# Performance work log

Hardware: AMD Instinct MI355X
Metric: run time of the kernel (lower is better)

Reference implementation:

```python
import jax, jax.numpy as jnp
import numpy as np

N = 50000      # nodes
E = 800000     # edges
P = 200000     # link pairs
D_IN = 128     # input_dim
F_NUM = 128    # filter_num
OUT = 2        # out_dim
K = 10         # APPNP propagation steps
ALPHA = 0.1    # teleport prob


def setup_inputs() -> dict:
    key = jax.random.key(0)
    ks = jax.random.split(key, 9)
    x = jax.random.normal(ks[0], (N, D_IN), dtype=jnp.float32)
    edge_index = jax.random.randint(ks[1], (2, E), 0, N)
    index = jax.random.randint(ks[2], (P, 2), 0, N)
    s1 = 1.0 / np.sqrt(D_IN)
    s2 = 1.0 / np.sqrt(F_NUM)
    s3 = 1.0 / np.sqrt(2 * F_NUM)
    W1 = jax.random.uniform(ks[3], (F_NUM, D_IN), minval=-s1, maxval=s1)
    b1 = jax.random.uniform(ks[4], (F_NUM,), minval=-s1, maxval=s1)
    W2 = jax.random.uniform(ks[5], (F_NUM, F_NUM), minval=-s2, maxval=s2)
    b2 = jax.random.uniform(ks[6], (F_NUM,), minval=-s2, maxval=s2)
    W3 = jax.random.uniform(ks[7], (OUT, 2 * F_NUM), minval=-s3, maxval=s3)
    b3 = jax.random.uniform(ks[8], (OUT,), minval=-s3, maxval=s3)
    return {"x": x, "edge_index": edge_index, "index": index,
            "W1": W1, "b1": b1, "W2": W2, "b2": b2, "W3": W3, "b3": b3}


def _gcn_norm(edge_index, num_nodes):
    # PyG gcn_norm: add self-loops, sym norm D^{-1/2} (A+I) D^{-1/2}
    src, dst = edge_index[0], edge_index[1]
    loop = jnp.arange(num_nodes, dtype=src.dtype)
    src = jnp.concatenate([src, loop])
    dst = jnp.concatenate([dst, loop])
    deg = jax.ops.segment_sum(jnp.ones_like(src, dtype=jnp.float32), dst,
                              num_segments=num_nodes)
    dinv = jnp.where(deg > 0, jax.lax.rsqrt(deg), 0.0)
    norm = dinv[src] * dinv[dst]  # [E+N]
    return src, dst, norm


def _appnp(x, src, dst, norm, num_nodes):
    # h_{k+1} = (1-alpha) * A_hat h_k + alpha * x0
    def step(h, _):
        agg = jax.ops.segment_sum(norm[:, None] * h[src], dst,
                                  num_segments=num_nodes)
        return (1.0 - ALPHA) * agg + ALPHA * x, None
    h, _ = jax.lax.scan(step, x, None, length=K)
    return h


def reference(x, edge_index, index, W1, b1, W2, b2, W3, b3):
    num_nodes = x.shape[0]
    src, dst, norm = _gcn_norm(edge_index, num_nodes)
    h = x @ W1.T + b1                      # [N, F]
    h = jax.nn.relu(_appnp(h, src, dst, norm, num_nodes))
    h = h @ W2.T + b2                      # [N, F]
    h = jax.nn.relu(_appnp(h, src, dst, norm, num_nodes))
    feat = jnp.concatenate([h[index[:, 0]], h[index[:, 1]]], axis=-1)  # [P, 2F]
    out = feat @ W3.T + b3                 # [P, OUT]
    return jax.nn.log_softmax(out, axis=1)
```

## Files before the change

### kernel.cpp

```cpp
#include <hip/hip_runtime.h>
#include <math.h>

#define NN 50000
#define NE 800000
#define NP 200000
#define NF 128
#define NEDGE_TOT (NE + NN)
#define NBLK 196

typedef __attribute__((ext_vector_type(8))) short short8;
typedef __attribute__((ext_vector_type(4))) float float4v;

__device__ __forceinline__ float bf_lo(unsigned u) { return __uint_as_float(u << 16); }
__device__ __forceinline__ float bf_hi(unsigned u) { return __uint_as_float(u & 0xffff0000u); }
__device__ __forceinline__ unsigned short f2bf(float f) {
    unsigned u = __float_as_uint(f);
    return (unsigned short)((u + 0x7fffu + ((u >> 16) & 1u)) >> 16);
}
__device__ __forceinline__ unsigned pack2bf(float a, float b) {
    return (unsigned)f2bf(a) | ((unsigned)f2bf(b) << 16);
}

__global__ __launch_bounds__(256) void init_cnt_k(int* __restrict__ cnt) {
    int i = blockIdx.x * 256 + threadIdx.x;
    if (i < NN) cnt[i] = 1;
}

__global__ __launch_bounds__(256) void count_k(const int* __restrict__ ei,
                                               int* __restrict__ cnt) {
    int e = blockIdx.x * 256 + threadIdx.x;
    if (e < NE) atomicAdd(&cnt[ei[NE + e]], 1);
}

__global__ __launch_bounds__(256) void scan_reduce_k(const int* __restrict__ cnt,
                                                     int* __restrict__ bsum,
                                                     float* __restrict__ dinv) {
    __shared__ int s[256];
    int t = threadIdx.x;
    int idx = blockIdx.x * 256 + t;
    int v = (idx < NN) ? cnt[idx] : 0;
    if (idx < NN) dinv[idx] = rsqrtf((float)v);
    s[t] = v;
    __syncthreads();
    for (int off = 128; off > 0; off >>= 1) {
        if (t < off) s[t] += s[t + off];
        __syncthreads();
    }
    if (t == 0) bsum[blockIdx.x] = s[0];
}

__global__ __launch_bounds__(256) void scan_bsums_k(const int* __restrict__ bsum,
                                                    int* __restrict__ boff) {
    __shared__ int s[256];
    int t = threadIdx.x;
    int v = (t < NBLK) ? bsum[t] : 0;
    s[t] = v;
    __syncthreads();
    for (int off = 1; off < 256; off <<= 1) {
        int add = (t >= off) ? s[t - off] : 0;
        __syncthreads();
        s[t] += add;
        __syncthreads();
    }
    if (t < NBLK) boff[t] = s[t] - v;
}

__global__ __launch_bounds__(256) void scan_down_k(const int* __restrict__ cnt,
                                                   const int* __restrict__ boff,
                                                   int* __restrict__ row_ptr,
                                                   int* __restrict__ wptr) {
    __shared__ int s[256];
    int t = threadIdx.x;
    int idx = blockIdx.x * 256 + t;
    int v = (idx < NN) ? cnt[idx] : 0;
    s[t] = v;
    __syncthreads();
    for (int off = 1; off < 256; off <<= 1) {
        int add = (t >= off) ? s[t - off] : 0;
        __syncthreads();
        s[t] += add;
        __syncthreads();
    }
    int excl = s[t] - v + boff[blockIdx.x];
    if (idx < NN) {
        row_ptr[idx] = excl;
        wptr[idx] = excl;
        if (idx == NN - 1) row_ptr[NN] = excl + v;
    }
}

__global__ __launch_bounds__(256) void scatter_k(const int* __restrict__ ei,
                                                 const float* __restrict__ dinv,
                                                 int* __restrict__ wptr,
                                                 int2* __restrict__ rec) {
    int e = blockIdx.x * 256 + threadIdx.x;
    if (e >= NEDGE_TOT) return;
    int s, d;
    if (e < NE) { s = ei[e]; d = ei[NE + e]; }
    else        { s = d = e - NE; }
    int pos = atomicAdd(&wptr[d], 1);
    int2 r;
    r.x = s;
    r.y = __float_as_int(dinv[s] * dinv[d]);
    rec[pos] = r;
}

__global__ __launch_bounds__(256) void cast_x_k(const float* __restrict__ x,
                                                unsigned short* __restrict__ Xb) {
    int t = blockIdx.x * 256 + threadIdx.x;
    if (t >= NN * 16) return;
    int i = t * 8;
    float4 f0 = *(const float4*)(x + i);
    float4 f1 = *(const float4*)(x + i + 4);
    uint4 q;
    q.x = pack2bf(f0.x, f0.y);
    q.y = pack2bf(f0.z, f0.w);
    q.z = pack2bf(f1.x, f1.y);
    q.w = pack2bf(f1.z, f1.w);
    *(uint4*)(Xb + i) = q;
}

__global__ __launch_bounds__(256) void cast_w_k(const float* __restrict__ W,
                                                unsigned short* __restrict__ Wb) {
    int t = blockIdx.x * 256 + threadIdx.x;
    if (t >= 128 * 128 / 8) return;
    int i = t * 8;
    float4 f0 = *(const float4*)(W + i);
    float4 f1 = *(const float4*)(W + i + 4);
    uint4 q;
    q.x = pack2bf(f0.x, f0.y);
    q.y = pack2bf(f0.z, f0.w);
    q.z = pack2bf(f1.x, f1.y);
    q.w = pack2bf(f1.z, f1.w);
    *(uint4*)(Wb + i) = q;
}

#define GPAD 136
__global__ __launch_bounds__(256) void gemm_mfma_k(const unsigned short* __restrict__ Xb,
                                                   const unsigned short* __restrict__ Wb,
                                                   const float* __restrict__ bias,
                                                   unsigned short* __restrict__ Yb,
                                                   int nrows) {
    __shared__ unsigned short sm[4 * 16 * GPAD];
    int wave = threadIdx.x >> 6, lane = threadIdx.x & 63;
    int rbase = blockIdx.x * 64 + wave * 16;
    if (rbase >= nrows) return;
    int quad = lane >> 4, mn = lane & 15;
    float4v acc[8];
#pragma unroll
    for (int ft = 0; ft < 8; ++ft) acc[ft] = (float4v){0.f, 0.f, 0.f, 0.f};
#pragma unroll
    for (int kb = 0; kb < 128; kb += 32) {
        short8 a = *(const short8*)(Xb + (size_t)(rbase + mn) * NF + kb + quad * 8);
#pragma unroll
        for (int ft = 0; ft < 8; ++ft) {
            short8 b = *(const short8*)(Wb + (size_t)(ft * 16 + mn) * NF + kb + quad * 8);
            acc[ft] = __builtin_amdgcn_mfma_f32_16x16x32_bf16(a, b, acc[ft], 0, 0, 0);
        }
    }
    unsigned short* smw = sm + wave * 16 * GPAD;
#pragma unroll
    for (int ft = 0; ft < 8; ++ft) {
        float bv = bias[ft * 16 + mn];
#pragma unroll
        for (int r = 0; r < 4; ++r)
            smw[(quad * 4 + r) * GPAD + ft * 16 + mn] = f2bf(acc[ft][r] + bv);
    }
    __syncthreads();
#pragma unroll
    for (int t = 0; t < 4; ++t) {
        int rl = t * 4 + quad;
        uint4 q = *(const uint4*)(smw + rl * GPAD + mn * 8);
        *(uint4*)(Yb + (size_t)(rbase + rl) * NF + mn * 8) = q;
    }
}

__global__ __launch_bounds__(256) void appnp4_k(const unsigned short* __restrict__ h,
                                                const unsigned short* __restrict__ x0,
                                                unsigned short* __restrict__ out,
                                                const int* __restrict__ row_ptr,
                                                const int2* __restrict__ rec,
                                                int relu, int proj,
                                                const float* __restrict__ W3,
                                                float4* __restrict__ puv) {
    int wid = (blockIdx.x * 256 + threadIdx.x) >> 6;
    int lane = threadIdx.x & 63;
    if (wid >= NN) return;
    int g = lane >> 4, li = lane & 15;
    int beg = row_ptr[wid], end = row_ptr[wid + 1];
    float a0 = 0.f, a1 = 0.f, a2 = 0.f, a3 = 0.f;
    float a4 = 0.f, a5 = 0.f, a6 = 0.f, a7 = 0.f;
    for (int e = beg; e < end; e += 64) {
        int m = end - e;
        if (m > 64) m = 64;
        int c = 0;
        float w = 0.f;
        if (lane < m) { int2 q = rec[e + lane]; c = q.x; w = __int_as_float(q.y); }
        for (int j = 0; j < m; j += 4) {
            int src = j + g;
            int cj = __shfl(c, src, 64);
            float wj = __shfl(w, src, 64);
            if (src < m) {
                uint4 q = *((const uint4*)(h + (size_t)cj * NF) + li);
                a0 += wj * bf_lo(q.x);
                a1 += wj * bf_hi(q.x);
                a2 += wj * bf_lo(q.y);
                a3 += wj * bf_hi(q.y);
                a4 += wj * bf_lo(q.z);
                a5 += wj * bf_hi(q.z);
                a6 += wj * bf_lo(q.w);
                a7 += wj * bf_hi(q.w);
            }
        }
    }
#pragma unroll
    for (int off = 16; off < 64; off <<= 1) {
        a0 += __shfl_xor(a0, off, 64);
        a1 += __shfl_xor(a1, off, 64);
        a2 += __shfl_xor(a2, off, 64);
        a3 += __shfl_xor(a3, off, 64);
        a4 += __shfl_xor(a4, off, 64);
        a5 += __shfl_xor(a5, off, 64);
        a6 += __shfl_xor(a6, off, 64);
        a7 += __shfl_xor(a7, off, 64);
    }
    if (g == 0) {
        uint4 xq = *((const uint4*)(x0 + (size_t)wid * NF) + li);
        float r0 = 0.9f * a0 + 0.1f * bf_lo(xq.x);
        float r1 = 0.9f * a1 + 0.1f * bf_hi(xq.x);
        float r2 = 0.9f * a2 + 0.1f * bf_lo(xq.y);
        float r3 = 0.9f * a3 + 0.1f * bf_hi(xq.y);
        float r4 = 0.9f * a4 + 0.1f * bf_lo(xq.z);
        float r5 = 0.9f * a5 + 0.1f * bf_hi(xq.z);
        float r6 = 0.9f * a6 + 0.1f * bf_lo(xq.w);
        float r7 = 0.9f * a7 + 0.1f * bf_hi(xq.w);
        if (relu) {
            r0 = fmaxf(r0, 0.f); r1 = fmaxf(r1, 0.f);
            r2 = fmaxf(r2, 0.f); r3 = fmaxf(r3, 0.f);
            r4 = fmaxf(r4, 0.f); r5 = fmaxf(r5, 0.f);
            r6 = fmaxf(r6, 0.f); r7 = fmaxf(r7, 0.f);
        }
        if (!proj) {
            uint4 oq;
            oq.x = pack2bf(r0, r1);
            oq.y = pack2bf(r2, r3);
            oq.z = pack2bf(r4, r5);
            oq.w = pack2bf(r6, r7);
            *((uint4*)(out + (size_t)wid * NF) + li) = oq;
        } else {
            int fb = li * 8;
            float4 wu0a = *(const float4*)(W3 + fb);
            float4 wu0b = *(const float4*)(W3 + fb + 4);
            float4 wv0a = *(const float4*)(W3 + 128 + fb);
            float4 wv0b = *(const float4*)(W3 + 128 + fb + 4);
            float4 wu1a = *(const float4*)(W3 + 256 + fb);
            float4 wu1b = *(const float4*)(W3 + 256 + fb + 4);
            float4 wv1a = *(const float4*)(W3 + 384 + fb);
            float4 wv1b = *(const float4*)(W3 + 384 + fb + 4);
            float du0 = r0 * wu0a.x + r1 * wu0a.y + r2 * wu0a.z + r3 * wu0a.w
                      + r4 * wu0b.x + r5 * wu0b.y + r6 * wu0b.z + r7 * wu0b.w;
            float du1 = r0 * wu1a.x + r1 * wu1a.y + r2 * wu1a.z + r3 * wu1a.w
                      + r4 * wu1b.x + r5 * wu1b.y + r6 * wu1b.z + r7 * wu1b.w;
            float dv0 = r0 * wv0a.x + r1 * wv0a.y + r2 * wv0a.z + r3 * wv0a.w
                      + r4 * wv0b.x + r5 * wv0b.y + r6 * wv0b.z + r7 * wv0b.w;
            float dv1 = r0 * wv1a.x + r1 * wv1a.y + r2 * wv1a.z + r3 * wv1a.w
                      + r4 * wv1b.x + r5 * wv1b.y + r6 * wv1b.z + r7 * wv1b.w;
#pragma unroll
            for (int off = 1; off < 16; off <<= 1) {
                du0 += __shfl_xor(du0, off, 64);
                du1 += __shfl_xor(du1, off, 64);
                dv0 += __shfl_xor(dv0, off, 64);
                dv1 += __shfl_xor(dv1, off, 64);
            }
            if (li == 0) puv[wid] = make_float4(du0, du1, dv0, dv1);
        }
    }
}

__global__ __launch_bounds__(256) void pair2_k(const float4* __restrict__ puv,
                                               const int2* __restrict__ index,
                                               const float* __restrict__ b3,
                                               float* __restrict__ outp) {
    int p = blockIdx.x * 256 + threadIdx.x;
    if (p >= NP) return;
    int2 uv = index[p];
    float4 a = puv[uv.x];
    float4 b = puv[uv.y];
    float s0 = a.x + b.z + b3[0];
    float s1 = a.y + b.w + b3[1];
    float m = fmaxf(s0, s1);
    float lse = m + logf(expf(s0 - m) + expf(s1 - m));
    *(float2*)(outp + (size_t)p * 2) = make_float2(s0 - lse, s1 - lse);
}

extern "C" void kernel_launch(void* const* d_in, const int* in_sizes, int n_in,
                              void* d_out, int out_size, void* d_ws, size_t ws_size,
                              hipStream_t stream) {
    const float* x  = (const float*)d_in[0];
    const int* ei   = (const int*)d_in[1];
    const int* idx  = (const int*)d_in[2];
    const float* W1 = (const float*)d_in[3];
    const float* b1 = (const float*)d_in[4];
    const float* W2 = (const float*)d_in[5];
    const float* b2 = (const float*)d_in[6];
    const float* W3 = (const float*)d_in[7];
    const float* b3 = (const float*)d_in[8];
    float* out = (float*)d_out;

    char* ws = (char*)d_ws;
    size_t off = 0;
    auto alloc = [&](size_t bytes) -> void* {
        void* p = ws + off;
        off = (off + bytes + 255) & ~(size_t)255;
        return p;
    };
    int*   cnt     = (int*)  alloc(NN * sizeof(int));
    float* dinv    = (float*)alloc(NN * sizeof(float));
    int*   row_ptr = (int*)  alloc((NN + 1) * sizeof(int));
    int*   wptr    = (int*)  alloc(NN * sizeof(int));
    int*   bsum    = (int*)  alloc(NBLK * sizeof(int));
    int*   boff    = (int*)  alloc(NBLK * sizeof(int));
    int2*  rec     = (int2*) alloc((size_t)NEDGE_TOT * sizeof(int2));
    float4* puv    = (float4*)alloc((size_t)NN * sizeof(float4));
    unsigned short* Xb  = (unsigned short*)alloc((size_t)NN * NF * 2);
    unsigned short* Wb1 = (unsigned short*)alloc(128 * 128 * 2);
    unsigned short* Wb2 = (unsigned short*)alloc(128 * 128 * 2);
    unsigned short* H0  = (unsigned short*)alloc((size_t)NN * NF * 2);
    unsigned short* HA  = (unsigned short*)alloc((size_t)NN * NF * 2);
    unsigned short* HB  = (unsigned short*)alloc((size_t)NN * NF * 2);

    const int gN    = (NN + 255) / 256;
    const int gE    = (NE + 255) / 256;
    const int gET   = (NEDGE_TOT + 255) / 256;
    const int gGemm = (NN + 63) / 64;
    const int gStep = (NN * 64 + 255) / 256;
    const int gPair = (NP + 255) / 256;

    cast_w_k<<<8, 256, 0, stream>>>(W1, Wb1);
    cast_w_k<<<8, 256, 0, stream>>>(W2, Wb2);
    cast_x_k<<<(NN * 16 + 255) / 256, 256, 0, stream>>>(x, Xb);
    init_cnt_k<<<gN, 256, 0, stream>>>(cnt);
    count_k<<<gE, 256, 0, stream>>>(ei, cnt);
    scan_reduce_k<<<NBLK, 256, 0, stream>>>(cnt, bsum, dinv);
    scan_bsums_k<<<1, 256, 0, stream>>>(bsum, boff);
    scan_down_k<<<NBLK, 256, 0, stream>>>(cnt, boff, row_ptr, wptr);
    scatter_k<<<gET, 256, 0, stream>>>(ei, dinv, wptr, rec);

    gemm_mfma_k<<<gGemm, 256, 0, stream>>>(Xb, Wb1, b1, H0, NN);
    {
        const unsigned short* cur = H0;
        for (int k = 0; k < 10; ++k) {
            unsigned short* dst = (k & 1) ? HB : HA;
            appnp4_k<<<gStep, 256, 0, stream>>>(cur, H0, dst, row_ptr, rec,
                                                (k == 9) ? 1 : 0, 0, W3, puv);
            cur = dst;
        }
    }
    gemm_mfma_k<<<gGemm, 256, 0, stream>>>(HB, Wb2, b2, H0, NN);
    {
        const unsigned short* cur = H0;
        for (int k = 0; k < 10; ++k) {
            unsigned short* dst = (k & 1) ? HB : HA;
            appnp4_k<<<gStep, 256, 0, stream>>>(cur, H0, dst, row_ptr, rec,
                                                (k == 9) ? 1 : 0,
                                                (k == 9) ? 1 : 0, W3, puv);
            cur = dst;
        }
    }
    pair2_k<<<gPair, 256, 0, stream>>>(puv, (const int2*)idx, b3, out);
}
```

Measured before the change: 909.7 us.

## Assign one 16-lane group per node in APPNP propagation with 4-way unrolled gathers

```diff
diff --git a/kernel.cpp b/kernel.cpp
--- a/kernel.cpp
+++ b/kernel.cpp
@@ -175,105 +175,112 @@
     }
 }
 
-__global__ __launch_bounds__(256) void appnp4_k(const unsigned short* __restrict__ h,
-                                                const unsigned short* __restrict__ x0,
-                                                unsigned short* __restrict__ out,
-                                                const int* __restrict__ row_ptr,
-                                                const int2* __restrict__ rec,
-                                                int relu, int proj,
-                                                const float* __restrict__ W3,
-                                                float4* __restrict__ puv) {
-    int wid = (blockIdx.x * 256 + threadIdx.x) >> 6;
-    int lane = threadIdx.x & 63;
-    if (wid >= NN) return;
-    int g = lane >> 4, li = lane & 15;
-    int beg = row_ptr[wid], end = row_ptr[wid + 1];
+__global__ __launch_bounds__(256) void appnp_g_k(const unsigned short* __restrict__ h,
+                                                 const unsigned short* __restrict__ x0,
+                                                 unsigned short* __restrict__ out,
+                                                 const int* __restrict__ row_ptr,
+                                                 const int2* __restrict__ rec,
+                                                 int relu, int proj,
+                                                 const float* __restrict__ W3,
+                                                 float4* __restrict__ puv) {
+    int node = (blockIdx.x * 256 + threadIdx.x) >> 4;
+    int li = threadIdx.x & 15;
+    if (node >= NN) return;
+    int gb = (threadIdx.x & 63) & ~15;
+    int beg = row_ptr[node], end = row_ptr[node + 1];
     float a0 = 0.f, a1 = 0.f, a2 = 0.f, a3 = 0.f;
     float a4 = 0.f, a5 = 0.f, a6 = 0.f, a7 = 0.f;
-    for (int e = beg; e < end; e += 64) {
+    for (int e = beg; e < end; e += 16) {
         int m = end - e;
-        if (m > 64) m = 64;
+        if (m > 16) m = 16;
         int c = 0;
         float w = 0.f;
-        if (lane < m) { int2 q = rec[e + lane]; c = q.x; w = __int_as_float(q.y); }
-        for (int j = 0; j < m; j += 4) {
-            int src = j + g;
-            int cj = __shfl(c, src, 64);
-            float wj = __shfl(w, src, 64);
-            if (src < m) {
-                uint4 q = *((const uint4*)(h + (size_t)cj * NF) + li);
-                a0 += wj * bf_lo(q.x);
-                a1 += wj * bf_hi(q.x);
-                a2 += wj * bf_lo(q.y);
-                a3 += wj * bf_hi(q.y);
-                a4 += wj * bf_lo(q.z);
-                a5 += wj * bf_hi(q.z);
-                a6 += wj * bf_lo(q.w);
-                a7 += wj * bf_hi(q.w);
-            }
-        }
-    }
-#pragma unroll
-    for (int off = 16; off < 64; off <<= 1) {
-        a0 += __shfl_xor(a0, off, 64);
-        a1 += __shfl_xor(a1, off, 64);
-        a2 += __shfl_xor(a2, off, 64);
-        a3 += __shfl_xor(a3, off, 64);
-        a4 += __shfl_xor(a4, off, 64);
-        a5 += __shfl_xor(a5, off, 64);
-        a6 += __shfl_xor(a6, off, 64);
-        a7 += __shfl_xor(a7, off, 64);
-    }
-    if (g == 0) {
-        uint4 xq = *((const uint4*)(x0 + (size_t)wid * NF) + li);
-        float r0 = 0.9f * a0 + 0.1f * bf_lo(xq.x);
-        float r1 = 0.9f * a1 + 0.1f * bf_hi(xq.x);
-        float r2 = 0.9f * a2 + 0.1f * bf_lo(xq.y);
-        float r3 = 0.9f * a3 + 0.1f * bf_hi(xq.y);
-        float r4 = 0.9f * a4 + 0.1f * bf_lo(xq.z);
-        float r5 = 0.9f * a5 + 0.1f * bf_hi(xq.z);
-        float r6 = 0.9f * a6 + 0.1f * bf_lo(xq.w);
-        float r7 = 0.9f * a7 + 0.1f * bf_hi(xq.w);
-        if (relu) {
-            r0 = fmaxf(r0, 0.f); r1 = fmaxf(r1, 0.f);
-            r2 = fmaxf(r2, 0.f); r3 = fmaxf(r3, 0.f);
-            r4 = fmaxf(r4, 0.f); r5 = fmaxf(r5, 0.f);
-            r6 = fmaxf(r6, 0.f); r7 = fmaxf(r7, 0.f);
-        }
-        if (!proj) {
-            uint4 oq;
-            oq.x = pack2bf(r0, r1);
-            oq.y = pack2bf(r2, r3);
-            oq.z = pack2bf(r4, r5);
-            oq.w = pack2bf(r6, r7);
-            *((uint4*)(out + (size_t)wid * NF) + li) = oq;
-        } else {
-            int fb = li * 8;
-            float4 wu0a = *(const float4*)(W3 + fb);
-            float4 wu0b = *(const float4*)(W3 + fb + 4);
-            float4 wv0a = *(const float4*)(W3 + 128 + fb);
-            float4 wv0b = *(const float4*)(W3 + 128 + fb + 4);
-            float4 wu1a = *(const float4*)(W3 + 256 + fb);
-            float4 wu1b = *(const float4*)(W3 + 256 + fb + 4);
-            float4 wv1a = *(const float4*)(W3 + 384 + fb);
-            float4 wv1b = *(const float4*)(W3 + 384 + fb + 4);
-            float du0 = r0 * wu0a.x + r1 * wu0a.y + r2 * wu0a.z + r3 * wu0a.w
-                      + r4 * wu0b.x + r5 * wu0b.y + r6 * wu0b.z + r7 * wu0b.w;
-            float du1 = r0 * wu1a.x + r1 * wu1a.y + r2 * wu1a.z + r3 * wu1a.w
-                      + r4 * wu1b.x + r5 * wu1b.y + r6 * wu1b.z + r7 * wu1b.w;
-            float dv0 = r0 * wv0a.x + r1 * wv0a.y + r2 * wv0a.z + r3 * wv0a.w
-                      + r4 * wv0b.x + r5 * wv0b.y + r6 * wv0b.z + r7 * wv0b.w;
-            float dv1 = r0 * wv1a.x + r1 * wv1a.y + r2 * wv1a.z + r3 * wv1a.w
-                      + r4 * wv1b.x + r5 * wv1b.y + r6 * wv1b.z + r7 * wv1b.w;
-#pragma unroll
-            for (int off = 1; off < 16; off <<= 1) {
-                du0 += __shfl_xor(du0, off, 64);
-                du1 += __shfl_xor(du1, off, 64);
-                dv0 += __shfl_xor(dv0, off, 64);
-                dv1 += __shfl_xor(dv1, off, 64);
-            }
-            if (li == 0) puv[wid] = make_float4(du0, du1, dv0, dv1);
-        }
+        if (li < m) { int2 q = rec[e + li]; c = q.x; w = __int_as_float(q.y); }
+        int j = 0;
+        for (; j + 4 <= m; j += 4) {
+            int c0 = __shfl(c, gb + j, 64),     c1 = __shfl(c, gb + j + 1, 64);
+            int c2 = __shfl(c, gb + j + 2, 64), c3 = __shfl(c, gb + j + 3, 64);
+            float w0 = __shfl(w, gb + j, 64),     w1 = __shfl(w, gb + j + 1, 64);
+            float w2 = __shfl(w, gb + j + 2, 64), w3 = __shfl(w, gb + j + 3, 64);
+            uint4 q0 = *((const uint4*)(h + (size_t)c0 * NF) + li);
+            uint4 q1 = *((const uint4*)(h + (size_t)c1 * NF) + li);
+            uint4 q2 = *((const uint4*)(h + (size_t)c2 * NF) + li);
+            uint4 q3 = *((const uint4*)(h + (size_t)c3 * NF) + li);
+            a0 += w0 * bf_lo(q0.x); a1 += w0 * bf_hi(q0.x);
+            a2 += w0 * bf_lo(q0.y); a3 += w0 * bf_hi(q0.y);
+            a4 += w0 * bf_lo(q0.z); a5 += w0 * bf_hi(q0.z);
+            a6 += w0 * bf_lo(q0.w); a7 += w0 * bf_hi(q0.w);
+            a0 += w1 * bf_lo(q1.x); a1 += w1 * bf_hi(q1.x);
+            a2 += w1 * bf_lo(q1.y); a3 += w1 * bf_hi(q1.y);
+            a4 += w1 * bf_lo(q1.z); a5 += w1 * bf_hi(q1.z);
+            a6 += w1 * bf_lo(q1.w); a7 += w1 * bf_hi(q1.w);
+            a0 += w2 * bf_lo(q2.x); a1 += w2 * bf_hi(q2.x);
+            a2 += w2 * bf_lo(q2.y); a3 += w2 * bf_hi(q2.y);
+            a4 += w2 * bf_lo(q2.z); a5 += w2 * bf_hi(q2.z);
+            a6 += w2 * bf_lo(q2.w); a7 += w2 * bf_hi(q2.w);
+            a0 += w3 * bf_lo(q3.x); a1 += w3 * bf_hi(q3.x);
+            a2 += w3 * bf_lo(q3.y); a3 += w3 * bf_hi(q3.y);
+            a4 += w3 * bf_lo(q3.z); a5 += w3 * bf_hi(q3.z);
+            a6 += w3 * bf_lo(q3.w); a7 += w3 * bf_hi(q3.w);
+        }
+        for (; j < m; ++j) {
+            int cj = __shfl(c, gb + j, 64);
+            float wj = __shfl(w, gb + j, 64);
+            uint4 q = *((const uint4*)(h + (size_t)cj * NF) + li);
+            a0 += wj * bf_lo(q.x); a1 += wj * bf_hi(q.x);
+            a2 += wj * bf_lo(q.y); a3 += wj * bf_hi(q.y);
+            a4 += wj * bf_lo(q.z); a5 += wj * bf_hi(q.z);
+            a6 += wj * bf_lo(q.w); a7 += wj * bf_hi(q.w);
+        }
+    }
+    uint4 xq = *((const uint4*)(x0 + (size_t)node * NF) + li);
+    float r0 = 0.9f * a0 + 0.1f * bf_lo(xq.x);
+    float r1 = 0.9f * a1 + 0.1f * bf_hi(xq.x);
+    float r2 = 0.9f * a2 + 0.1f * bf_lo(xq.y);
+    float r3 = 0.9f * a3 + 0.1f * bf_hi(xq.y);
+    float r4 = 0.9f * a4 + 0.1f * bf_lo(xq.z);
+    float r5 = 0.9f * a5 + 0.1f * bf_hi(xq.z);
+    float r6 = 0.9f * a6 + 0.1f * bf_lo(xq.w);
+    float r7 = 0.9f * a7 + 0.1f * bf_hi(xq.w);
+    if (relu) {
+        r0 = fmaxf(r0, 0.f); r1 = fmaxf(r1, 0.f);
+        r2 = fmaxf(r2, 0.f); r3 = fmaxf(r3, 0.f);
+        r4 = fmaxf(r4, 0.f); r5 = fmaxf(r5, 0.f);
+        r6 = fmaxf(r6, 0.f); r7 = fmaxf(r7, 0.f);
+    }
+    if (!proj) {
+        uint4 oq;
+        oq.x = pack2bf(r0, r1);
+        oq.y = pack2bf(r2, r3);
+        oq.z = pack2bf(r4, r5);
+        oq.w = pack2bf(r6, r7);
+        *((uint4*)(out + (size_t)node * NF) + li) = oq;
+    } else {
+        int fb = li * 8;
+        float4 wu0a = *(const float4*)(W3 + fb);
+        float4 wu0b = *(const float4*)(W3 + fb + 4);
+        float4 wv0a = *(const float4*)(W3 + 128 + fb);
+        float4 wv0b = *(const float4*)(W3 + 128 + fb + 4);
+        float4 wu1a = *(const float4*)(W3 + 256 + fb);
+        float4 wu1b = *(const float4*)(W3 + 256 + fb + 4);
+        float4 wv1a = *(const float4*)(W3 + 384 + fb);
+        float4 wv1b = *(const float4*)(W3 + 384 + fb + 4);
+        float du0 = r0 * wu0a.x + r1 * wu0a.y + r2 * wu0a.z + r3 * wu0a.w
+                  + r4 * wu0b.x + r5 * wu0b.y + r6 * wu0b.z + r7 * wu0b.w;
+        float du1 = r0 * wu1a.x + r1 * wu1a.y + r2 * wu1a.z + r3 * wu1a.w
+                  + r4 * wu1b.x + r5 * wu1b.y + r6 * wu1b.z + r7 * wu1b.w;
+        float dv0 = r0 * wv0a.x + r1 * wv0a.y + r2 * wv0a.z + r3 * wv0a.w
+                  + r4 * wv0b.x + r5 * wv0b.y + r6 * wv0b.z + r7 * wv0b.w;
+        float dv1 = r0 * wv1a.x + r1 * wv1a.y + r2 * wv1a.z + r3 * wv1a.w
+                  + r4 * wv1b.x + r5 * wv1b.y + r6 * wv1b.z + r7 * wv1b.w;
+#pragma unroll
+        for (int off = 1; off < 16; off <<= 1) {
+            du0 += __shfl_xor(du0, off, 64);
+            du1 += __shfl_xor(du1, off, 64);
+            dv0 += __shfl_xor(dv0, off, 64);
+            dv1 += __shfl_xor(dv1, off, 64);
+        }
+        if (li == 0) puv[node] = make_float4(du0, du1, dv0, dv1);
     }
 }
 
@@ -333,7 +340,7 @@
     const int gE    = (NE + 255) / 256;
     const int gET   = (NEDGE_TOT + 255) / 256;
     const int gGemm = (NN + 63) / 64;
-    const int gStep = (NN * 64 + 255) / 256;
+    const int gStep = (NN * 16 + 255) / 256;
     const int gPair = (NP + 255) / 256;
 
     cast_w_k<<<8, 256, 0, stream>>>(W1, Wb1);
@@ -351,8 +358,8 @@
         const unsigned short* cur = H0;
         for (int k = 0; k < 10; ++k) {
             unsigned short* dst = (k & 1) ? HB : HA;
-            appnp4_k<<<gStep, 256, 0, stream>>>(cur, H0, dst, row_ptr, rec,
-                                                (k == 9) ? 1 : 0, 0, W3, puv);
+            appnp_g_k<<<gStep, 256, 0, stream>>>(cur, H0, dst, row_ptr, rec,
+                                                 (k == 9) ? 1 : 0, 0, W3, puv);
             cur = dst;
         }
     }
@@ -361,9 +368,9 @@
         const unsigned short* cur = H0;
         for (int k = 0; k < 10; ++k) {
             unsigned short* dst = (k & 1) ? HB : HA;
-            appnp4_k<<<gStep, 256, 0, stream>>>(cur, H0, dst, row_ptr, rec,
-                                                (k == 9) ? 1 : 0,
-                                                (k == 9) ? 1 : 0, W3, puv);
+            appnp_g_k<<<gStep, 256, 0, stream>>>(cur, H0, dst, row_ptr, rec,
+                                                 (k == 9) ? 1 : 0,
+                                                 (k == 9) ? 1 : 0, W3, puv);
             cur = dst;
         }
     }
```

Result: faster. 841.6 us (-7.5%).
